# Optimization experiments

Hardware: AMD Instinct MI355X
Metric: run time of the kernel (lower is better)

Reference implementation:

```python
import jax, jax.numpy as jnp
import numpy as np

IN, HID, B = 512, 512, 16384

def _linear_params(key, fan_in, fan_out, bias_const=None):
    kw, kb = jax.random.split(key)
    bound = 1.0 / np.sqrt(fan_in)
    W = jax.random.uniform(kw, (fan_out, fan_in), jnp.float32, -bound, bound)
    if bias_const is None:
        b = jax.random.uniform(kb, (fan_out,), jnp.float32, -bound, bound)
    else:
        b = jnp.full((fan_out,), bias_const, jnp.float32)
    return W, b

def setup_inputs() -> dict:
    key = jax.random.key(0)
    ks = jax.random.split(key, 11)
    x = jax.random.normal(ks[0], (B, IN), jnp.float32)
    h = jax.random.normal(ks[1], (B, HID), jnp.float32)
    c = jax.random.normal(ks[2], (B, HID), jnp.float32)
    Wxi, bxi = _linear_params(ks[3], IN, HID)
    Wxo, bxo = _linear_params(ks[4], IN, HID)
    Wxf, bxf = _linear_params(ks[5], IN, HID, bias_const=1.0)
    Wxg, bxg = _linear_params(ks[6], IN, HID)
    Whi, bhi = _linear_params(ks[7], HID, HID)
    Who, bho = _linear_params(ks[8], HID, HID)
    Whf, bhf = _linear_params(ks[9], HID, HID, bias_const=1.0)
    Whg, bhg = _linear_params(ks[10], HID, HID)
    return dict(x=x, h=h, c=c,
                Wxi=Wxi, bxi=bxi, Wxo=Wxo, bxo=bxo, Wxf=Wxf, bxf=bxf, Wxg=Wxg, bxg=bxg,
                Whi=Whi, bhi=bhi, Who=Who, bho=bho, Whf=Whf, bhf=bhf, Whg=Whg, bhg=bhg)

def reference(x, h, c,
              Wxi, bxi, Wxo, bxo, Wxf, bxf, Wxg, bxg,
              Whi, bhi, Who, bho, Whf, bhf, Whg, bhg):
    # Batch the four input projections and four hidden projections into two GEMMs.
    Wx = jnp.concatenate([Wxi, Wxg, Wxf, Wxo], axis=0)   # [4H, IN]
    Wh = jnp.concatenate([Whi, Whg, Whf, Who], axis=0)   # [4H, HID]
    bx = jnp.concatenate([bxi, bxg, bxf, bxo], axis=0)
    bh = jnp.concatenate([bhi, bhg, bhf, bho], axis=0)
    gates = x @ Wx.T + h @ Wh.T + bx + bh                 # [B, 4H]
    i_pre, g_pre, f_pre, o_pre = jnp.split(gates, 4, axis=1)
    i = jax.nn.sigmoid(i_pre)
    g = jnp.tanh(g_pre)
    f = jax.nn.sigmoid(f_pre)
    o = jax.nn.sigmoid(o_pre)
    c_new = f * c + i * g
    h_new = o * jnp.tanh(c_new)
    return (h_new, c_new)
```

## Files before the change

### kernel.cpp

```cpp
#include <hip/hip_runtime.h>
#include <cstdint>
#include <cstddef>


#define BATCH 16384
#define KDIM  1024
#define NPK   2048
#define HIDN  512

#define BM 256
#define BN 256
#define BK 64
#define NT (KDIM / BK)

typedef __bf16 bf16x8 __attribute__((ext_vector_type(8)));
typedef float  f32x4  __attribute__((ext_vector_type(4)));

__device__ __forceinline__ unsigned short f2bf(float f) {
  unsigned int u = __builtin_bit_cast(unsigned int, f);
  u += 0x7fffu + ((u >> 16) & 1u);
  return (unsigned short)(u >> 16);
}

__device__ __forceinline__ float fast_sigmoid(float x) {
  return __builtin_amdgcn_rcpf(1.0f + __expf(-x));
}
__device__ __forceinline__ float fast_tanh(float x) {
  return 1.0f - 2.0f * __builtin_amdgcn_rcpf(1.0f + __expf(2.0f * x));
}

__device__ __forceinline__ void gload_lds16(const void* gp, void* lds_wave_base) {
  auto g = (const __attribute__((address_space(1))) unsigned int*)(unsigned long long)gp;
  auto l = (__attribute__((address_space(3))) unsigned int*)
           (unsigned int)(unsigned long long)lds_wave_base;
  __builtin_amdgcn_global_load_lds(g, l, 16, 0, 0);
}

__global__ __launch_bounds__(256) void pack_a(const float* __restrict__ x,
                                              const float* __restrict__ h,
                                              unsigned short* __restrict__ A) {
  int c = blockIdx.x * 256 + threadIdx.x;
  int idx = c << 3;
  int b = idx >> 10;
  int k = idx & 1023;
  const float* src = (k < 512) ? (x + (size_t)b * 512 + k)
                               : (h + (size_t)b * 512 + (k - 512));
  float4 lo = ((const float4*)src)[0];
  float4 hi = ((const float4*)src)[1];
  union { unsigned short s[8]; uint4 u; } o;
  o.s[0]=f2bf(lo.x); o.s[1]=f2bf(lo.y); o.s[2]=f2bf(lo.z); o.s[3]=f2bf(lo.w);
  o.s[4]=f2bf(hi.x); o.s[5]=f2bf(hi.y); o.s[6]=f2bf(hi.z); o.s[7]=f2bf(hi.w);
  ((uint4*)A)[c] = o.u;
}

struct GatePtrs {
  const float* wx[4];
  const float* wh[4];
  const float* bx[4];
  const float* bh[4];
};

__global__ __launch_bounds__(256) void pack_w(GatePtrs P,
                                              unsigned short* __restrict__ W,
                                              float* __restrict__ bias) {
  int c = blockIdx.x * 256 + threadIdx.x;
  int r = c >> 7;
  int k = (c & 127) << 3;
  int b    = r >> 7;
  int rem  = r & 127;
  int wn   = (rem >> 6) & 1;
  int gate = (rem >> 4) & 3;
  int jl   = rem & 15;
  int j = b * 32 + wn * 16 + jl;
  const float* src = (k < 512) ? (P.wx[gate] + (size_t)j * 512 + k)
                               : (P.wh[gate] + (size_t)j * 512 + (k - 512));
  float4 lo = ((const float4*)src)[0];
  float4 hi = ((const float4*)src)[1];
  union { unsigned short s[8]; uint4 u; } o;
  o.s[0]=f2bf(lo.x); o.s[1]=f2bf(lo.y); o.s[2]=f2bf(lo.z); o.s[3]=f2bf(lo.w);
  o.s[4]=f2bf(hi.x); o.s[5]=f2bf(hi.y); o.s[6]=f2bf(hi.z); o.s[7]=f2bf(hi.w);
  ((uint4*)W)[c] = o.u;
  if ((c & 127) == 0) bias[r] = P.bx[gate][j] + P.bh[gate][j];
}


__global__ __launch_bounds__(512, 2) void lstm_gemm(
    const unsigned short* __restrict__ A,
    const unsigned short* __restrict__ W,
    const float* __restrict__ bias,
    const float* __restrict__ Cin,
    float* __restrict__ Hout,
    float* __restrict__ Cout) {
  __shared__ __align__(16) unsigned short lds[2 * 32768];

  const int tid  = threadIdx.x;
  const int lane = tid & 63;
  const int wv   = tid >> 6;
  const int wm   = wv >> 2;
  const int wn   = wv & 3;

  const int lin = blockIdx.x;
  const int xcd = lin & 7;
  const int idx = lin >> 3;
  const int bn  = idx & 7;
  const int bm  = (idx >> 3) * 8 + xcd;

  const int srow = lane >> 2;
  const int scol = (((lane & 3) ^ ((srow >> 1) & 3)) << 3);
  const unsigned short* gA = A + (size_t)(bm * 256 + wv * 32 + srow) * KDIM + scol;
  const unsigned short* gB = W + (size_t)(bn * 256 + wv * 32 + srow) * KDIM + scol;
  const int lA = wv * 1024;

#define REG_A(b, c) ((b) * 32768 + (c) * 8192)
#define REG_B(b, c) ((b) * 32768 + 16384 + (c) * 8192)

#define STAGE_A(b, c, tt) do {                                      \
    const unsigned short* s_ = gA + (tt) * 64 + (c) * 32;           \
    gload_lds16(s_,            &lds[REG_A(b, c) + lA]);             \
    gload_lds16(s_ + 16 * KDIM, &lds[REG_A(b, c) + lA + 512]);      \
  } while (0)
#define STAGE_B(b, c, tt) do {                                      \
    const unsigned short* s_ = gB + (tt) * 64 + (c) * 32;           \
    gload_lds16(s_,            &lds[REG_B(b, c) + lA]);             \
    gload_lds16(s_ + 16 * KDIM, &lds[REG_B(b, c) + lA + 512]);      \
  } while (0)

  const int lrow = lane & 15;
  const int kg   = (((lane >> 4) ^ ((lrow >> 1) & 3)) << 3);
  const int aoff = wm * 4096 + lrow * 32 + kg;
  const int boff = wn * 2048 + lrow * 32 + kg;

  f32x4 acc[8][4] = {};
  bf16x8 af[4], bfr[4];

#define LOAD_AF(b, c, h) do {                                                  \
    _Pragma("unroll")                                                          \
    for (int mi = 0; mi < 4; ++mi)                                             \
      af[mi] = *reinterpret_cast<const bf16x8*>(                               \
          &lds[REG_A(b, c) + aoff + (h) * 2048 + mi * 512]);                   \
  } while (0)
#define LOAD_BF(b, c) do {                                                     \
    _Pragma("unroll")                                                          \
    for (int ni = 0; ni < 4; ++ni)                                             \
      bfr[ni] = *reinterpret_cast<const bf16x8*>(                              \
          &lds[REG_B(b, c) + boff + ni * 512]);                                \
  } while (0)
#define MFMA_BLK(h) do {                                                       \
    __builtin_amdgcn_s_setprio(1);                                             \
    _Pragma("unroll")                                                          \
    for (int mi = 0; mi < 4; ++mi)                                             \
      _Pragma("unroll")                                                        \
      for (int ni = 0; ni < 4; ++ni)                                           \
        acc[(h) * 4 + mi][ni] = __builtin_amdgcn_mfma_f32_16x16x32_bf16(       \
            af[mi], bfr[ni], acc[(h) * 4 + mi][ni], 0, 0, 0);                  \
    __builtin_amdgcn_s_setprio(0);                                             \
  } while (0)

#define BAR()  __builtin_amdgcn_s_barrier()
#define SCB()  __builtin_amdgcn_sched_barrier(0)
#define WAIT_LGKM0() do { asm volatile("s_waitcnt lgkmcnt(0)" ::: "memory"); SCB(); } while (0)

  STAGE_B(0, 0, 0); STAGE_A(0, 0, 0); STAGE_B(0, 1, 0); STAGE_A(0, 1, 0);
  STAGE_B(1, 0, 1); STAGE_A(1, 0, 1); STAGE_B(1, 1, 1);
  asm volatile("s_waitcnt vmcnt(6)" ::: "memory");
  BAR(); SCB();

#pragma unroll 2
  for (int t = 0; t < NT; ++t) {
    const int cur = t & 1;
    const int nxt = cur ^ 1;
    const int t1 = (t + 1 < NT) ? t + 1 : NT - 1;
    const int t2 = (t + 2 < NT) ? t + 2 : NT - 1;
    LOAD_AF(cur, 0, 0); LOAD_BF(cur, 0);
    STAGE_A(nxt, 1, t1);
    BAR(); WAIT_LGKM0();
    MFMA_BLK(0);
    BAR(); SCB();
    LOAD_AF(cur, 0, 1);
    STAGE_B(cur, 0, t2);
    BAR(); WAIT_LGKM0();
    MFMA_BLK(1);
    BAR(); SCB();
    LOAD_AF(cur, 1, 0); LOAD_BF(cur, 1);
    STAGE_A(cur, 0, t2);
    BAR(); WAIT_LGKM0();
    MFMA_BLK(0);
    BAR(); SCB();
    LOAD_AF(cur, 1, 1);
    STAGE_B(cur, 1, t2);
    BAR(); WAIT_LGKM0();
    MFMA_BLK(1);
    asm volatile("s_waitcnt vmcnt(6)" ::: "memory");
    BAR(); SCB();
  }
  asm volatile("s_waitcnt vmcnt(0)" ::: "memory");

  const int jl = lane & 15;
  const int rq = (lane >> 4) << 2;
  const int j  = (bn * 2 + (wn >> 1)) * 32 + (wn & 1) * 16 + jl;
  float bv[4];
#pragma unroll
  for (int ni = 0; ni < 4; ++ni)
    bv[ni] = bias[bn * 256 + wn * 64 + ni * 16 + jl];

#pragma unroll
  for (int mi = 0; mi < 8; ++mi) {
    const int row0 = bm * 256 + wm * 128 + (mi >> 2) * 64 + (mi & 3) * 16 + rq;
#pragma unroll
    for (int r = 0; r < 4; ++r) {
      int row = row0 + r;
      float iv = fast_sigmoid(acc[mi][0][r] + bv[0]);
      float gv = fast_tanh   (acc[mi][1][r] + bv[1]);
      float fv = fast_sigmoid(acc[mi][2][r] + bv[2]);
      float ov = fast_sigmoid(acc[mi][3][r] + bv[3]);
      float cold = Cin[(size_t)row * HIDN + j];
      float cnew = fv * cold + iv * gv;
      Hout[(size_t)row * HIDN + j] = ov * fast_tanh(cnew);
      Cout[(size_t)row * HIDN + j] = cnew;
    }
  }
}


extern "C" void kernel_launch(void* const* d_in, const int* in_sizes, int n_in,
                              void* d_out, int out_size, void* d_ws, size_t ws_size,
                              hipStream_t stream) {
  const float* x   = (const float*)d_in[0];
  const float* h   = (const float*)d_in[1];
  const float* c   = (const float*)d_in[2];
  const float* Wxi = (const float*)d_in[3];  const float* bxi = (const float*)d_in[4];
  const float* Wxo = (const float*)d_in[5];  const float* bxo = (const float*)d_in[6];
  const float* Wxf = (const float*)d_in[7];  const float* bxf = (const float*)d_in[8];
  const float* Wxg = (const float*)d_in[9];  const float* bxg = (const float*)d_in[10];
  const float* Whi = (const float*)d_in[11]; const float* bhi = (const float*)d_in[12];
  const float* Who = (const float*)d_in[13]; const float* bho = (const float*)d_in[14];
  const float* Whf = (const float*)d_in[15]; const float* bhf = (const float*)d_in[16];
  const float* Whg = (const float*)d_in[17]; const float* bhg = (const float*)d_in[18];

  char* ws = (char*)d_ws;
  unsigned short* Apack = (unsigned short*)ws;
  unsigned short* Wpack = (unsigned short*)(ws + (size_t)BATCH * KDIM * 2);
  float* biasp = (float*)(ws + (size_t)BATCH * KDIM * 2 + (size_t)NPK * KDIM * 2);

  pack_a<<<(BATCH * KDIM / 8) / 256, 256, 0, stream>>>(x, h, Apack);

  GatePtrs P;
  P.wx[0] = Wxi; P.wx[1] = Wxg; P.wx[2] = Wxf; P.wx[3] = Wxo;
  P.wh[0] = Whi; P.wh[1] = Whg; P.wh[2] = Whf; P.wh[3] = Who;
  P.bx[0] = bxi; P.bx[1] = bxg; P.bx[2] = bxf; P.bx[3] = bxo;
  P.bh[0] = bhi; P.bh[1] = bhg; P.bh[2] = bhf; P.bh[3] = bho;
  pack_w<<<(NPK * KDIM / 8) / 256, 256, 0, stream>>>(P, Wpack, biasp);

  float* Hout = (float*)d_out;
  float* Cout = Hout + (size_t)BATCH * HIDN;
  lstm_gemm<<<dim3((BATCH / BM) * (NPK / BN)), 512, 0, stream>>>(
      Apack, Wpack, biasp, c, Hout, Cout);
}
```

Measured before the change: 248.1 us.

## Double-buffer A fragments in registers to overlap LDS reads with MFMA

```diff
diff --git a/kernel.cpp b/kernel.cpp
--- a/kernel.cpp
+++ b/kernel.cpp
@@ -131,39 +131,41 @@
   const int boff = wn * 2048 + lrow * 32 + kg;
 
   f32x4 acc[8][4] = {};
-  bf16x8 af[4], bfr[4];
-
-#define LOAD_AF(b, c, h) do {                                                  \
+  bf16x8 afA[4], afB[4];
+  bf16x8 bfr[4];
+
+#define LOAD_AF_TO(dst, b, c, h) do {                                          \
     _Pragma("unroll")                                                          \
     for (int mi = 0; mi < 4; ++mi)                                             \
-      af[mi] = *reinterpret_cast<const bf16x8*>(                               \
+      dst[mi] = *reinterpret_cast<const bf16x8*>(                              \
           &lds[REG_A(b, c) + aoff + (h) * 2048 + mi * 512]);                   \
   } while (0)
-#define LOAD_BF(b, c) do {                                                     \
+#define LOAD_BF_TO(dst, b, c) do {                                             \
     _Pragma("unroll")                                                          \
     for (int ni = 0; ni < 4; ++ni)                                             \
-      bfr[ni] = *reinterpret_cast<const bf16x8*>(                              \
+      dst[ni] = *reinterpret_cast<const bf16x8*>(                              \
           &lds[REG_B(b, c) + boff + ni * 512]);                                \
   } while (0)
-#define MFMA_BLK(h) do {                                                       \
+#define MFMA_BLK(h, aset) do {                                                 \
     __builtin_amdgcn_s_setprio(1);                                             \
     _Pragma("unroll")                                                          \
     for (int mi = 0; mi < 4; ++mi)                                             \
       _Pragma("unroll")                                                        \
       for (int ni = 0; ni < 4; ++ni)                                           \
         acc[(h) * 4 + mi][ni] = __builtin_amdgcn_mfma_f32_16x16x32_bf16(       \
-            af[mi], bfr[ni], acc[(h) * 4 + mi][ni], 0, 0, 0);                  \
+            aset[mi], bfr[ni], acc[(h) * 4 + mi][ni], 0, 0, 0);                \
     __builtin_amdgcn_s_setprio(0);                                             \
   } while (0)
 
 #define BAR()  __builtin_amdgcn_s_barrier()
 #define SCB()  __builtin_amdgcn_sched_barrier(0)
-#define WAIT_LGKM0() do { asm volatile("s_waitcnt lgkmcnt(0)" ::: "memory"); SCB(); } while (0)
 
   STAGE_B(0, 0, 0); STAGE_A(0, 0, 0); STAGE_B(0, 1, 0); STAGE_A(0, 1, 0);
   STAGE_B(1, 0, 1); STAGE_A(1, 0, 1); STAGE_B(1, 1, 1);
   asm volatile("s_waitcnt vmcnt(6)" ::: "memory");
   BAR(); SCB();
+  LOAD_AF_TO(afA, 0, 0, 0);
+  LOAD_BF_TO(bfr, 0, 0);
 
 #pragma unroll 2
   for (int t = 0; t < NT; ++t) {
@@ -171,27 +173,29 @@
     const int nxt = cur ^ 1;
     const int t1 = (t + 1 < NT) ? t + 1 : NT - 1;
     const int t2 = (t + 2 < NT) ? t + 2 : NT - 1;
-    LOAD_AF(cur, 0, 0); LOAD_BF(cur, 0);
+    LOAD_AF_TO(afB, cur, 0, 1);
     STAGE_A(nxt, 1, t1);
-    BAR(); WAIT_LGKM0();
-    MFMA_BLK(0);
-    BAR(); SCB();
-    LOAD_AF(cur, 0, 1);
+    MFMA_BLK(0, afA);
+    SCB();
+    BAR();
+    LOAD_AF_TO(afA, cur, 1, 0);
     STAGE_B(cur, 0, t2);
-    BAR(); WAIT_LGKM0();
-    MFMA_BLK(1);
-    BAR(); SCB();
-    LOAD_AF(cur, 1, 0); LOAD_BF(cur, 1);
+    MFMA_BLK(1, afB);
+    SCB();
+    LOAD_BF_TO(bfr, cur, 1);
+    BAR();
+    LOAD_AF_TO(afB, cur, 1, 1);
     STAGE_A(cur, 0, t2);
-    BAR(); WAIT_LGKM0();
-    MFMA_BLK(0);
-    BAR(); SCB();
-    LOAD_AF(cur, 1, 1);
+    MFMA_BLK(0, afA);
+    SCB();
+    BAR();
     STAGE_B(cur, 1, t2);
-    BAR(); WAIT_LGKM0();
-    MFMA_BLK(1);
     asm volatile("s_waitcnt vmcnt(6)" ::: "memory");
-    BAR(); SCB();
+    if (t < NT - 1) LOAD_AF_TO(afA, nxt, 0, 0);
+    MFMA_BLK(1, afB);
+    SCB();
+    if (t < NT - 1) LOAD_BF_TO(bfr, nxt, 0);
+    BAR();
   }
   asm volatile("s_waitcnt vmcnt(0)" ::: "memory");
 
```

After: 245.2 us. Within noise of the previous version (-1.2%).
